# Optimization experiments

Hardware: AMD Instinct MI355X
Metric: run time of the kernel (lower is better)

Reference implementation:

```python
import jax, jax.numpy as jnp
import numpy as np

N_NODES = 10000
N_EDGES = 640000
D_IN = 128
D_HID = 128
# torch rrelu in eval mode == leaky_relu with slope (lower+upper)/2 = (1/8+1/3)/2
RRELU_SLOPE = 11.0 / 48.0


def setup_inputs() -> dict:
    key = jax.random.key(0)
    k1, k2, k3, k4, k5, k6 = jax.random.split(key, 6)
    node_h = jax.random.normal(k1, (N_NODES, D_IN), dtype=jnp.float32)
    edge_h = jax.random.normal(k2, (N_EDGES, D_IN), dtype=jnp.float32)
    norm = jax.random.uniform(k3, (N_EDGES, 1), dtype=jnp.float32)
    W = jax.random.normal(k4, (D_HID, 2 * D_IN), dtype=jnp.float32) * (1.0 / np.sqrt(2 * D_IN))
    src = jax.random.randint(k5, (N_EDGES,), 0, N_NODES, dtype=jnp.int64)
    dst = jax.random.randint(k6, (N_EDGES,), 0, N_NODES, dtype=jnp.int64)
    return {"node_h": node_h, "edge_h": edge_h, "norm": norm, "W": W, "src": src, "dst": dst}


def reference(node_h, edge_h, norm, W, src, dst):
    # Linear on cat([src_h, edge_h]) == src_h @ W_src.T + edge_h @ W_edge.T
    W_src = W[:, :D_IN]   # [H, D]
    W_edge = W[:, D_IN:]  # [H, D]
    # Project node features once per node, then gather (saves E-vs-N FLOPs).
    proj_nodes = jnp.einsum('nd,hd->nh', node_h, W_src)          # [N, H]
    msg = (proj_nodes[src] + jnp.einsum('ed,hd->eh', edge_h, W_edge)) * norm  # [E, H]
    h = jax.ops.segment_sum(msg, dst, num_segments=N_NODES)     # [N, H]
    # rrelu (eval mode): leaky relu with deterministic mean slope
    return jnp.where(h >= 0, h, RRELU_SLOPE * h)
```

## Files before the change

kernel.cpp:

```cpp
#include <hip/hip_runtime.h>

#define NN 10000
#define NE 640000
#define D  128
#define SLOPE 0.22916666666666666f

__global__ void hist_kernel(const int* __restrict__ dst, int* __restrict__ cnt) {
    int e = blockIdx.x * 256 + threadIdx.x;
    if (e < NE) atomicAdd(&cnt[dst[e]], 1);
}

__global__ __launch_bounds__(1024) void scan_kernel(const int* __restrict__ cnt,
                                                    int* __restrict__ cur) {
    __shared__ int sums[1024];
    int t = threadIdx.x;
    int base = t * 10;
    int local[10];
    int s = 0;
    #pragma unroll
    for (int i = 0; i < 10; ++i) {
        int v = (base + i < NN) ? cnt[base + i] : 0;
        local[i] = s; s += v;
    }
    sums[t] = s;
    __syncthreads();
    for (int off = 1; off < 1024; off <<= 1) {
        int v = (t >= off) ? sums[t - off] : 0;
        __syncthreads();
        sums[t] += v;
        __syncthreads();
    }
    int prev = sums[t] - s;
    #pragma unroll
    for (int i = 0; i < 10; ++i)
        if (base + i < NN) cur[base + i] = prev + local[i];
}

__global__ void scatter_kernel(const int* __restrict__ dst, int* __restrict__ cur,
                               int* __restrict__ order) {
    int e = blockIdx.x * 256 + threadIdx.x;
    if (e < NE) {
        int p = atomicAdd(&cur[dst[e]], 1);
        order[p] = e;
    }
}

__global__ __launch_bounds__(256) void agg_kernel(
    const float* __restrict__ node_h, const float* __restrict__ edge_h,
    const float* __restrict__ nrm, const int* __restrict__ src,
    const int* __restrict__ order, const int* __restrict__ cur,
    float* __restrict__ agg) {
    int t = threadIdx.x;
    int d = blockIdx.x * 4 + (t >> 6);
    int lane = t & 63;
    int start = (d == 0) ? 0 : cur[d - 1];
    int end = cur[d];
    int half = lane >> 5;
    int c = (lane & 31) * 4;

    float4 acc = {0.f, 0.f, 0.f, 0.f};

    int j = start;
    int e0 = 0, s0 = 0, e1 = 0, s1 = 0;
    float w0 = 0.f, w1 = 0.f;
    if (j < end)     { e0 = order[j];     s0 = src[e0]; w0 = nrm[e0]; }
    if (j + 1 < end) { e1 = order[j + 1]; s1 = src[e1]; w1 = nrm[e1]; }

    while (j + 1 < end) {
        const float* p0 = half ? &edge_h[(size_t)e0 * D + c] : &node_h[(size_t)s0 * D + c];
        const float* p1 = half ? &edge_h[(size_t)e1 * D + c] : &node_h[(size_t)s1 * D + c];
        float4 v0 = *(const float4*)p0;
        float4 v1 = *(const float4*)p1;
        int jn = j + 2;
        int en0 = 0, sn0 = 0, en1 = 0, sn1 = 0;
        float wn0 = 0.f, wn1 = 0.f;
        if (jn < end)     { en0 = order[jn];     sn0 = src[en0]; wn0 = nrm[en0]; }
        if (jn + 1 < end) { en1 = order[jn + 1]; sn1 = src[en1]; wn1 = nrm[en1]; }
        acc.x += w0 * v0.x; acc.y += w0 * v0.y; acc.z += w0 * v0.z; acc.w += w0 * v0.w;
        acc.x += w1 * v1.x; acc.y += w1 * v1.y; acc.z += w1 * v1.z; acc.w += w1 * v1.w;
        e0 = en0; s0 = sn0; w0 = wn0;
        e1 = en1; s1 = sn1; w1 = wn1;
        j = jn;
    }
    if (j < end) {
        const float* p0 = half ? &edge_h[(size_t)e0 * D + c] : &node_h[(size_t)s0 * D + c];
        float4 v0 = *(const float4*)p0;
        acc.x += w0 * v0.x; acc.y += w0 * v0.y; acc.z += w0 * v0.z; acc.w += w0 * v0.w;
    }
    *(float4*)&agg[(size_t)d * 256 + half * 128 + c] = acc;
}

#define TN 32
#define LDA 34
#define LDWT 136

__global__ __launch_bounds__(256) void gemm_kernel(
    const float* __restrict__ agg, const float* __restrict__ W,
    float* __restrict__ out) {
    __shared__ float sAT[256 * LDA];
    __shared__ float sWT[32 * LDWT];
    int t = threadIdx.x;
    int n0 = blockIdx.x * TN;

    {
        int n = t >> 3, kg = (t & 7) * 32;
        bool ok = (n0 + n) < NN;
        const float* srcp = &agg[(size_t)(n0 + n) * 256 + kg];
        #pragma unroll
        for (int j = 0; j < 32; j += 4) {
            float4 v = ok ? *(const float4*)&srcp[j] : float4{0.f, 0.f, 0.f, 0.f};
            sAT[(kg + j + 0) * LDA + n] = v.x;
            sAT[(kg + j + 1) * LDA + n] = v.y;
            sAT[(kg + j + 2) * LDA + n] = v.z;
            sAT[(kg + j + 3) * LDA + n] = v.w;
        }
    }

    int n2 = (t >> 4) * 2;
    int h0 = (t & 15) * 4;
    float acc[2][8];
    #pragma unroll
    for (int i = 0; i < 2; ++i)
        #pragma unroll
        for (int j = 0; j < 8; ++j) acc[i][j] = 0.f;

    for (int kc = 0; kc < 256; kc += 32) {
        __syncthreads();
        {
            int h = t >> 1, kl0 = (t & 1) * 16;
            const float* wp = &W[(size_t)h * 256 + kc + kl0];
            #pragma unroll
            for (int j = 0; j < 16; j += 4) {
                float4 v = *(const float4*)&wp[j];
                sWT[(kl0 + j + 0) * LDWT + h] = v.x;
                sWT[(kl0 + j + 1) * LDWT + h] = v.y;
                sWT[(kl0 + j + 2) * LDWT + h] = v.z;
                sWT[(kl0 + j + 3) * LDWT + h] = v.w;
            }
        }
        __syncthreads();
        #pragma unroll
        for (int kl = 0; kl < 32; ++kl) {
            int k = kc + kl;
            float2 a01 = *(const float2*)&sAT[k * LDA + n2];
            const float* wr = &sWT[kl * LDWT];
            float4 wA = *(const float4*)&wr[h0];
            float4 wB = *(const float4*)&wr[64 + h0];
            acc[0][0] += a01.x * wA.x; acc[0][1] += a01.x * wA.y;
            acc[0][2] += a01.x * wA.z; acc[0][3] += a01.x * wA.w;
            acc[0][4] += a01.x * wB.x; acc[0][5] += a01.x * wB.y;
            acc[0][6] += a01.x * wB.z; acc[0][7] += a01.x * wB.w;
            acc[1][0] += a01.y * wA.x; acc[1][1] += a01.y * wA.y;
            acc[1][2] += a01.y * wA.z; acc[1][3] += a01.y * wA.w;
            acc[1][4] += a01.y * wB.x; acc[1][5] += a01.y * wB.y;
            acc[1][6] += a01.y * wB.z; acc[1][7] += a01.y * wB.w;
        }
    }

    #pragma unroll
    for (int i = 0; i < 2; ++i) {
        int n = n0 + n2 + i;
        if (n < NN) {
            float4 o1, o2;
            o1.x = acc[i][0] >= 0.f ? acc[i][0] : SLOPE * acc[i][0];
            o1.y = acc[i][1] >= 0.f ? acc[i][1] : SLOPE * acc[i][1];
            o1.z = acc[i][2] >= 0.f ? acc[i][2] : SLOPE * acc[i][2];
            o1.w = acc[i][3] >= 0.f ? acc[i][3] : SLOPE * acc[i][3];
            o2.x = acc[i][4] >= 0.f ? acc[i][4] : SLOPE * acc[i][4];
            o2.y = acc[i][5] >= 0.f ? acc[i][5] : SLOPE * acc[i][5];
            o2.z = acc[i][6] >= 0.f ? acc[i][6] : SLOPE * acc[i][6];
            o2.w = acc[i][7] >= 0.f ? acc[i][7] : SLOPE * acc[i][7];
            *(float4*)&out[(size_t)n * D + h0] = o1;
            *(float4*)&out[(size_t)n * D + 64 + h0] = o2;
        }
    }
}

extern "C" void kernel_launch(void* const* d_in, const int* in_sizes, int n_in,
                              void* d_out, int out_size, void* d_ws, size_t ws_size,
                              hipStream_t stream) {
    const float* node_h = (const float*)d_in[0];
    const float* edge_h = (const float*)d_in[1];
    const float* nrm    = (const float*)d_in[2];
    const float* W      = (const float*)d_in[3];
    const int*   src    = (const int*)d_in[4];
    const int*   dst    = (const int*)d_in[5];
    float* out = (float*)d_out;

    float* agg  = (float*)d_ws;
    int*  order = (int*)((char*)d_ws + (size_t)NN * 256 * 4);
    int*  cnt   = order + NE;
    int*  cur   = cnt + NN;

    hipMemsetAsync(cnt, 0, (size_t)NN * sizeof(int), stream);
    hist_kernel<<<NE / 256, 256, 0, stream>>>(dst, cnt);
    scan_kernel<<<1, 1024, 0, stream>>>(cnt, cur);
    scatter_kernel<<<NE / 256, 256, 0, stream>>>(dst, cur, order);
    agg_kernel<<<NN / 4, 256, 0, stream>>>(node_h, edge_h, nrm, src, order, cur, agg);
    gemm_kernel<<<(NN + TN - 1) / TN, 256, 0, stream>>>(agg, W, out);
}
```

Measured before the change: 609.0 us.

## Pre-sort edge metadata in scatter, deepen gather prefetch, retile GEMM with pre-transposed W

The scatter pass now writes (edge id, src) pairs and norm values in dst-sorted order, so the aggregation loop reads contiguous metadata instead of making dependent indirect loads through order, src and nrm. The aggregation loop fetches four edges per iteration and prefetches the next four to raise memory-level parallelism. W is transposed once by a new small kernel, and the GEMM switches to 16-row tiles with contiguous shared-memory weight loads to get more blocks. The cost is extra workspace, an extra launch, and more scatter-side writes.

```diff
diff --git a/kernel.cpp b/kernel.cpp
--- a/kernel.cpp
+++ b/kernel.cpp
@@ -4,6 +4,12 @@
 #define NE 640000
 #define D  128
 #define SLOPE 0.22916666666666666f
+
+__global__ void wtrans_kernel(const float* __restrict__ W, float* __restrict__ WT) {
+    int i = blockIdx.x * 256 + threadIdx.x;
+    int h = i >> 8, k = i & 255;
+    WT[k * 128 + h] = W[i];
+}
 
 __global__ void hist_kernel(const int* __restrict__ dst, int* __restrict__ cnt) {
     int e = blockIdx.x * 256 + threadIdx.x;
@@ -36,20 +42,21 @@
         if (base + i < NN) cur[base + i] = prev + local[i];
 }
 
-__global__ void scatter_kernel(const int* __restrict__ dst, int* __restrict__ cur,
-                               int* __restrict__ order) {
+__global__ void scatter_kernel(const int* __restrict__ dst, const int* __restrict__ src,
+                               const float* __restrict__ nrm, int* __restrict__ cur,
+                               int2* __restrict__ meta, float* __restrict__ nrmS) {
     int e = blockIdx.x * 256 + threadIdx.x;
     if (e < NE) {
         int p = atomicAdd(&cur[dst[e]], 1);
-        order[p] = e;
+        meta[p] = make_int2(e, src[e]);
+        nrmS[p] = nrm[e];
     }
 }
 
 __global__ __launch_bounds__(256) void agg_kernel(
     const float* __restrict__ node_h, const float* __restrict__ edge_h,
-    const float* __restrict__ nrm, const int* __restrict__ src,
-    const int* __restrict__ order, const int* __restrict__ cur,
-    float* __restrict__ agg) {
+    const int2* __restrict__ meta, const float* __restrict__ nrmS,
+    const int* __restrict__ cur, float* __restrict__ agg) {
     int t = threadIdx.x;
     int d = blockIdx.x * 4 + (t >> 6);
     int lane = t & 63;
@@ -60,55 +67,59 @@
 
     float4 acc = {0.f, 0.f, 0.f, 0.f};
 
-    int j = start;
-    int e0 = 0, s0 = 0, e1 = 0, s1 = 0;
-    float w0 = 0.f, w1 = 0.f;
-    if (j < end)     { e0 = order[j];     s0 = src[e0]; w0 = nrm[e0]; }
-    if (j + 1 < end) { e1 = order[j + 1]; s1 = src[e1]; w1 = nrm[e1]; }
-
-    while (j + 1 < end) {
-        const float* p0 = half ? &edge_h[(size_t)e0 * D + c] : &node_h[(size_t)s0 * D + c];
-        const float* p1 = half ? &edge_h[(size_t)e1 * D + c] : &node_h[(size_t)s1 * D + c];
-        float4 v0 = *(const float4*)p0;
-        float4 v1 = *(const float4*)p1;
-        int jn = j + 2;
-        int en0 = 0, sn0 = 0, en1 = 0, sn1 = 0;
-        float wn0 = 0.f, wn1 = 0.f;
-        if (jn < end)     { en0 = order[jn];     sn0 = src[en0]; wn0 = nrm[en0]; }
-        if (jn + 1 < end) { en1 = order[jn + 1]; sn1 = src[en1]; wn1 = nrm[en1]; }
-        acc.x += w0 * v0.x; acc.y += w0 * v0.y; acc.z += w0 * v0.z; acc.w += w0 * v0.w;
-        acc.x += w1 * v1.x; acc.y += w1 * v1.y; acc.z += w1 * v1.z; acc.w += w1 * v1.w;
-        e0 = en0; s0 = sn0; w0 = wn0;
-        e1 = en1; s1 = sn1; w1 = wn1;
-        j = jn;
-    }
-    if (j < end) {
-        const float* p0 = half ? &edge_h[(size_t)e0 * D + c] : &node_h[(size_t)s0 * D + c];
-        float4 v0 = *(const float4*)p0;
-        acc.x += w0 * v0.x; acc.y += w0 * v0.y; acc.z += w0 * v0.z; acc.w += w0 * v0.w;
+    if (start < end) {
+        int2 m[4]; float w[4];
+        #pragma unroll
+        for (int i = 0; i < 4; ++i) {
+            int idx = (start + i < end) ? start + i : end - 1;
+            m[i] = meta[idx];
+            w[i] = (start + i < end) ? nrmS[idx] : 0.f;
+        }
+        for (int j = start; j < end; ) {
+            int2 cm[4]; float cw[4];
+            #pragma unroll
+            for (int i = 0; i < 4; ++i) { cm[i] = m[i]; cw[i] = w[i]; }
+            int jn = j + 4;
+            if (jn < end) {
+                #pragma unroll
+                for (int i = 0; i < 4; ++i) {
+                    int idx = (jn + i < end) ? jn + i : end - 1;
+                    m[i] = meta[idx];
+                    w[i] = (jn + i < end) ? nrmS[idx] : 0.f;
+                }
+            }
+            #pragma unroll
+            for (int i = 0; i < 4; ++i) {
+                const float* p = half ? &edge_h[(size_t)cm[i].x * D + c]
+                                      : &node_h[(size_t)cm[i].y * D + c];
+                float4 v = *(const float4*)p;
+                acc.x += cw[i] * v.x; acc.y += cw[i] * v.y;
+                acc.z += cw[i] * v.z; acc.w += cw[i] * v.w;
+            }
+            j = jn;
+        }
     }
     *(float4*)&agg[(size_t)d * 256 + half * 128 + c] = acc;
 }
 
-#define TN 32
-#define LDA 34
-#define LDWT 136
+#define TN  16
+#define LDA 18
 
 __global__ __launch_bounds__(256) void gemm_kernel(
-    const float* __restrict__ agg, const float* __restrict__ W,
+    const float* __restrict__ agg, const float* __restrict__ WT,
     float* __restrict__ out) {
     __shared__ float sAT[256 * LDA];
-    __shared__ float sWT[32 * LDWT];
+    __shared__ float sW[32 * 128];
     int t = threadIdx.x;
     int n0 = blockIdx.x * TN;
 
     {
-        int n = t >> 3, kg = (t & 7) * 32;
+        int n = t & 15, kg = (t >> 4) * 16;
         bool ok = (n0 + n) < NN;
-        const float* srcp = &agg[(size_t)(n0 + n) * 256 + kg];
+        const float* sp = &agg[(size_t)(n0 + n) * 256 + kg];
         #pragma unroll
-        for (int j = 0; j < 32; j += 4) {
-            float4 v = ok ? *(const float4*)&srcp[j] : float4{0.f, 0.f, 0.f, 0.f};
+        for (int j = 0; j < 16; j += 4) {
+            float4 v = ok ? *(const float4*)&sp[j] : float4{0.f, 0.f, 0.f, 0.f};
             sAT[(kg + j + 0) * LDA + n] = v.x;
             sAT[(kg + j + 1) * LDA + n] = v.y;
             sAT[(kg + j + 2) * LDA + n] = v.z;
@@ -116,44 +127,30 @@
         }
     }
 
-    int n2 = (t >> 4) * 2;
-    int h0 = (t & 15) * 4;
-    float acc[2][8];
-    #pragma unroll
-    for (int i = 0; i < 2; ++i)
-        #pragma unroll
-        for (int j = 0; j < 8; ++j) acc[i][j] = 0.f;
+    int n2 = (t >> 5) * 2;
+    int h0 = (t & 31) * 4;
+    float acc[2][4] = {{0.f,0.f,0.f,0.f},{0.f,0.f,0.f,0.f}};
 
     for (int kc = 0; kc < 256; kc += 32) {
         __syncthreads();
         {
-            int h = t >> 1, kl0 = (t & 1) * 16;
-            const float* wp = &W[(size_t)h * 256 + kc + kl0];
-            #pragma unroll
-            for (int j = 0; j < 16; j += 4) {
-                float4 v = *(const float4*)&wp[j];
-                sWT[(kl0 + j + 0) * LDWT + h] = v.x;
-                sWT[(kl0 + j + 1) * LDWT + h] = v.y;
-                sWT[(kl0 + j + 2) * LDWT + h] = v.z;
-                sWT[(kl0 + j + 3) * LDWT + h] = v.w;
-            }
+            const float4* wp = (const float4*)&WT[kc * 128];
+            float4* dp = (float4*)sW;
+            dp[t]       = wp[t];
+            dp[t + 256] = wp[t + 256];
+            dp[t + 512] = wp[t + 512];
+            dp[t + 768] = wp[t + 768];
         }
         __syncthreads();
         #pragma unroll
         for (int kl = 0; kl < 32; ++kl) {
             int k = kc + kl;
-            float2 a01 = *(const float2*)&sAT[k * LDA + n2];
-            const float* wr = &sWT[kl * LDWT];
-            float4 wA = *(const float4*)&wr[h0];
-            float4 wB = *(const float4*)&wr[64 + h0];
-            acc[0][0] += a01.x * wA.x; acc[0][1] += a01.x * wA.y;
-            acc[0][2] += a01.x * wA.z; acc[0][3] += a01.x * wA.w;
-            acc[0][4] += a01.x * wB.x; acc[0][5] += a01.x * wB.y;
-            acc[0][6] += a01.x * wB.z; acc[0][7] += a01.x * wB.w;
-            acc[1][0] += a01.y * wA.x; acc[1][1] += a01.y * wA.y;
-            acc[1][2] += a01.y * wA.z; acc[1][3] += a01.y * wA.w;
-            acc[1][4] += a01.y * wB.x; acc[1][5] += a01.y * wB.y;
-            acc[1][6] += a01.y * wB.z; acc[1][7] += a01.y * wB.w;
+            float2 a = *(const float2*)&sAT[k * LDA + n2];
+            float4 w = *(const float4*)&sW[kl * 128 + h0];
+            acc[0][0] += a.x * w.x; acc[0][1] += a.x * w.y;
+            acc[0][2] += a.x * w.z; acc[0][3] += a.x * w.w;
+            acc[1][0] += a.y * w.x; acc[1][1] += a.y * w.y;
+            acc[1][2] += a.y * w.z; acc[1][3] += a.y * w.w;
         }
     }
 
@@ -161,17 +158,12 @@
     for (int i = 0; i < 2; ++i) {
         int n = n0 + n2 + i;
         if (n < NN) {
-            float4 o1, o2;
-            o1.x = acc[i][0] >= 0.f ? acc[i][0] : SLOPE * acc[i][0];
-            o1.y = acc[i][1] >= 0.f ? acc[i][1] : SLOPE * acc[i][1];
-            o1.z = acc[i][2] >= 0.f ? acc[i][2] : SLOPE * acc[i][2];
-            o1.w = acc[i][3] >= 0.f ? acc[i][3] : SLOPE * acc[i][3];
-            o2.x = acc[i][4] >= 0.f ? acc[i][4] : SLOPE * acc[i][4];
-            o2.y = acc[i][5] >= 0.f ? acc[i][5] : SLOPE * acc[i][5];
-            o2.z = acc[i][6] >= 0.f ? acc[i][6] : SLOPE * acc[i][6];
-            o2.w = acc[i][7] >= 0.f ? acc[i][7] : SLOPE * acc[i][7];
-            *(float4*)&out[(size_t)n * D + h0] = o1;
-            *(float4*)&out[(size_t)n * D + 64 + h0] = o2;
+            float4 o;
+            o.x = acc[i][0] >= 0.f ? acc[i][0] : SLOPE * acc[i][0];
+            o.y = acc[i][1] >= 0.f ? acc[i][1] : SLOPE * acc[i][1];
+            o.z = acc[i][2] >= 0.f ? acc[i][2] : SLOPE * acc[i][2];
+            o.w = acc[i][3] >= 0.f ? acc[i][3] : SLOPE * acc[i][3];
+            *(float4*)&out[(size_t)n * D + h0] = o;
         }
     }
 }
@@ -187,15 +179,19 @@
     const int*   dst    = (const int*)d_in[5];
     float* out = (float*)d_out;
 
-    float* agg  = (float*)d_ws;
-    int*  order = (int*)((char*)d_ws + (size_t)NN * 256 * 4);
-    int*  cnt   = order + NE;
-    int*  cur   = cnt + NN;
+    char* p = (char*)d_ws;
+    float* agg  = (float*)p;              p += (size_t)NN * 256 * 4;
+    int2*  meta = (int2*)p;               p += (size_t)NE * 8;
+    float* nrmS = (float*)p;              p += (size_t)NE * 4;
+    float* WT   = (float*)p;              p += (size_t)256 * 128 * 4;
+    int*   cnt  = (int*)p;                p += (size_t)NN * 4;
+    int*   cur  = (int*)p;
 
     hipMemsetAsync(cnt, 0, (size_t)NN * sizeof(int), stream);
+    wtrans_kernel<<<128, 256, 0, stream>>>(W, WT);
     hist_kernel<<<NE / 256, 256, 0, stream>>>(dst, cnt);
     scan_kernel<<<1, 1024, 0, stream>>>(cnt, cur);
-    scatter_kernel<<<NE / 256, 256, 0, stream>>>(dst, cur, order);
-    agg_kernel<<<NN / 4, 256, 0, stream>>>(node_h, edge_h, nrm, src, order, cur, agg);
-    gemm_kernel<<<(NN + TN - 1) / TN, 256, 0, stream>>>(agg, W, out);
+    scatter_kernel<<<NE / 256, 256, 0, stream>>>(dst, src, nrm, cur, meta, nrmS);
+    agg_kernel<<<NN / 4, 256, 0, stream>>>(node_h, edge_h, meta, nrmS, cur, agg);
+    gemm_kernel<<<(NN + TN - 1) / TN, 256, 0, stream>>>(agg, WT, out);
 }
```

New measurement: 581.2 us. 1.05x faster.
